# Kernel optimization log

Hardware: AMD Instinct MI355X
Metric: run time of the kernel (lower is better)

The kernel has to match this reference:

```python
import jax, jax.numpy as jnp
import numpy as np

EPS = 1e-5  # torch.nn.LayerNorm default
NUM_HEADS = 8


def _layernorm(x, g, b):
    mu = jnp.mean(x, axis=-1, keepdims=True)
    var = jnp.mean((x - mu) ** 2, axis=-1, keepdims=True)
    return (x - mu) * jax.lax.rsqrt(var + EPS) * g + b


def setup_inputs() -> dict:
    key = jax.random.key(0)
    ks = jax.random.split(key, 8)
    B, S, D = 4, 2048, 512
    scale = 0.02
    return {
        'x': jax.random.normal(ks[0], (B, S, D), dtype=jnp.float32),
        'gene_types': jax.random.randint(ks[1], (B, S), 0, 2),
        'tf_g': jnp.ones((D,), jnp.float32), 'tf_b': jnp.zeros((D,), jnp.float32),
        'tg_g': jnp.ones((D,), jnp.float32), 'tg_b': jnp.zeros((D,), jnp.float32),
        'in_proj_w': jax.random.normal(ks[2], (3 * D, D), dtype=jnp.float32) * scale,
        'in_proj_b': jnp.zeros((3 * D,), jnp.float32),
        'out_proj_w': jax.random.normal(ks[3], (D, D), dtype=jnp.float32) * scale,
        'out_proj_b': jnp.zeros((D,), jnp.float32),
        'w1': jax.random.normal(ks[4], (D // 2, D), dtype=jnp.float32) * scale,
        'b1': jnp.zeros((D // 2,), jnp.float32),
        'w2': jax.random.normal(ks[5], (1, D // 2), dtype=jnp.float32) * scale,
        'b2': jnp.zeros((1,), jnp.float32),
    }


def reference(x, gene_types, tf_g, tf_b, tg_g, tg_b,
              in_proj_w, in_proj_b, out_proj_w, out_proj_b,
              w1, b1, w2, b2):
    B, S, D = x.shape
    H = NUM_HEADS
    HD = D // H
    # --- vectorized per-token conditional LayerNorm (gene_type 0 -> tf, 1 -> target, else passthrough) ---
    gt = gene_types[..., None]
    xn = jnp.where(gt == 0, _layernorm(x, tf_g, tf_b),
                   jnp.where(gt == 1, _layernorm(x, tg_g, tg_b), x))
    # --- multi-head self-attention (torch MultiheadAttention, batch_first) ---
    qkv = xn @ in_proj_w.T + in_proj_b            # [B,S,3D]
    q, k, v = jnp.split(qkv, 3, axis=-1)
    to_heads = lambda t: t.reshape(B, S, H, HD).transpose(0, 2, 1, 3)  # [B,H,S,HD]
    q, k, v = to_heads(q), to_heads(k), to_heads(v)
    scores = jnp.einsum('bhqd,bhkd->bhqk', q, k) / jnp.sqrt(jnp.float32(HD))
    attn = jax.nn.softmax(scores, axis=-1)
    o = jnp.einsum('bhqk,bhkd->bhqd', attn, v)
    o = o.transpose(0, 2, 1, 3).reshape(B, S, D)
    o = o @ out_proj_w.T + out_proj_b
    xr = xn + o                                    # residual
    # --- regulatory strength gate: Linear -> SiLU -> Linear -> Sigmoid ---
    h = jax.nn.silu(xr @ w1.T + b1)                # [B,S,D/2]
    strength = jax.nn.sigmoid(h @ w2.T + b2)       # [B,S,1]
    return xr * strength
```

## Files before the change

kernel.cpp:

```cpp
#include <hip/hip_runtime.h>

typedef __bf16 bf16;
typedef __bf16 bf16x4_t __attribute__((ext_vector_type(4)));
typedef __bf16 bf16x8_t __attribute__((ext_vector_type(8)));
typedef float f32x4_t __attribute__((ext_vector_type(4)));

#define MFMA16(a, b, c) __builtin_amdgcn_mfma_f32_16x16x32_bf16(a, b, c, 0, 0, 0)

static __device__ __forceinline__ f32x4_t mfma_k16(bf16x4_t a, bf16x4_t b, f32x4_t c) {
#if __has_builtin(__builtin_amdgcn_mfma_f32_16x16x16bf16_1k)
    typedef short s16x4_t __attribute__((ext_vector_type(4)));
    return __builtin_amdgcn_mfma_f32_16x16x16bf16_1k(
        __builtin_bit_cast(s16x4_t, a), __builtin_bit_cast(s16x4_t, b), c, 0, 0, 0);
#else
    bf16x8_t az = {}, bz = {};
    az[0] = a[0]; az[1] = a[1]; az[2] = a[2]; az[3] = a[3];
    bz[0] = b[0]; bz[1] = b[1]; bz[2] = b[2]; bz[3] = b[3];
    return MFMA16(az, bz, c);
#endif
}

__global__ __launch_bounds__(256) void castln_k(const float* __restrict__ Wqkv,
                                                const float* __restrict__ Wout,
                                                const float* __restrict__ W1,
                                                bf16* __restrict__ wq,
                                                bf16* __restrict__ wo,
                                                bf16* __restrict__ w1b,
                                                const float* __restrict__ x,
                                                const int* __restrict__ gt,
                                                const float* __restrict__ tfg,
                                                const float* __restrict__ tfb,
                                                const float* __restrict__ tgg,
                                                const float* __restrict__ tgb,
                                                bf16* __restrict__ xn) {
    if (blockIdx.x < 4608) {
        int i = blockIdx.x * 256 + threadIdx.x;
        if (i < 786432) wq[i] = (bf16)Wqkv[i];
        else if (i < 1048576) wo[i - 786432] = (bf16)Wout[i - 786432];
        else if (i < 1179648) w1b[i - 1048576] = (bf16)W1[i - 1048576];
        return;
    }
    int wid = threadIdx.x >> 6, lane = threadIdx.x & 63;
    int t = (blockIdx.x - 4608) * 4 + wid;
    const float4* xr = (const float4*)(x + (size_t)t * 512);
    float4 a = xr[lane * 2], b = xr[lane * 2 + 1];
    float s = (a.x + a.y) + (a.z + a.w) + (b.x + b.y) + (b.z + b.w);
    float sq = a.x * a.x + a.y * a.y + a.z * a.z + a.w * a.w +
               b.x * b.x + b.y * b.y + b.z * b.z + b.w * b.w;
    for (int m = 1; m < 64; m <<= 1) {
        s += __shfl_xor(s, m, 64);
        sq += __shfl_xor(sq, m, 64);
    }
    float mean = s * (1.f / 512.f);
    float var = fmaxf(sq * (1.f / 512.f) - mean * mean, 0.f);
    float rstd = rsqrtf(var + 1e-5f);
    int g = gt[t];
    float4 o0, o1;
    if (g < 2) {
        const float4* gp = (const float4*)(g ? tgg : tfg);
        const float4* bp = (const float4*)(g ? tgb : tfb);
        float4 g0 = gp[lane * 2], g1 = gp[lane * 2 + 1];
        float4 b0 = bp[lane * 2], b1 = bp[lane * 2 + 1];
        o0.x = (a.x - mean) * rstd * g0.x + b0.x;
        o0.y = (a.y - mean) * rstd * g0.y + b0.y;
        o0.z = (a.z - mean) * rstd * g0.z + b0.z;
        o0.w = (a.w - mean) * rstd * g0.w + b0.w;
        o1.x = (b.x - mean) * rstd * g1.x + b1.x;
        o1.y = (b.y - mean) * rstd * g1.y + b1.y;
        o1.z = (b.z - mean) * rstd * g1.z + b1.z;
        o1.w = (b.w - mean) * rstd * g1.w + b1.w;
    } else {
        o0 = a; o1 = b;
    }
    bf16* xo = xn + (size_t)t * 512 + lane * 8;
    bf16x4_t p0, p1;
    p0[0] = (bf16)o0.x; p0[1] = (bf16)o0.y; p0[2] = (bf16)o0.z; p0[3] = (bf16)o0.w;
    p1[0] = (bf16)o1.x; p1[1] = (bf16)o1.y; p1[2] = (bf16)o1.z; p1[3] = (bf16)o1.w;
    *(bf16x4_t*)xo = p0;
    *(bf16x4_t*)(xo + 4) = p1;
}

__global__ __launch_bounds__(256) void gemmqkv_k(const bf16* __restrict__ A,
                                                 const bf16* __restrict__ B,
                                                 const float* __restrict__ bias,
                                                 bf16* __restrict__ q,
                                                 bf16* __restrict__ kk,
                                                 bf16* __restrict__ vt) {
    int m0 = blockIdx.x * 128, n0 = blockIdx.y * 128;
    int tid = threadIdx.x;
    int lane = tid & 63, w = tid >> 6;
    int quad = lane >> 4, l15 = lane & 15;
    int wm = (w >> 1) * 64, wn = (w & 1) * 64;
    __shared__ bf16 As[128 * 72];
    __shared__ bf16 Bs[128 * 72];
    f32x4_t acc[4][4] = {};
    int srow = tid >> 3, ssub = tid & 7;
    const bf16* Ab = A + (size_t)(m0 + srow) * 512 + ssub * 8;
    const bf16* Bb = B + (size_t)(n0 + srow) * 512 + ssub * 8;
    uint4 pa[4], pb[4];
    auto gload = [&](int s) {
        int k0 = s * 64;
#pragma unroll
        for (int i = 0; i < 4; ++i) {
            pa[i] = *(const uint4*)(Ab + (size_t)(i * 32) * 512 + k0);
            pb[i] = *(const uint4*)(Bb + (size_t)(i * 32) * 512 + k0);
        }
    };
    auto sstore = [&]() {
#pragma unroll
        for (int i = 0; i < 4; ++i) {
            *(uint4*)&As[(i * 32 + srow) * 72 + ssub * 8] = pa[i];
            *(uint4*)&Bs[(i * 32 + srow) * 72 + ssub * 8] = pb[i];
        }
    };
    gload(0);
    sstore();
    for (int s = 0; s < 8; ++s) {
        __syncthreads();
        if (s < 7) gload(s + 1);
#pragma unroll
        for (int ks = 0; ks < 2; ++ks) {
            bf16x8_t af[4], bfr[4];
            int koff = ks * 32 + quad * 8;
#pragma unroll
            for (int mt = 0; mt < 4; ++mt)
                af[mt] = *(const bf16x8_t*)&As[(wm + mt * 16 + l15) * 72 + koff];
#pragma unroll
            for (int nt = 0; nt < 4; ++nt)
                bfr[nt] = *(const bf16x8_t*)&Bs[(wn + nt * 16 + l15) * 72 + koff];
#pragma unroll
            for (int mt = 0; mt < 4; ++mt)
#pragma unroll
                for (int nt = 0; nt < 4; ++nt)
                    acc[mt][nt] = MFMA16(af[mt], bfr[nt], acc[mt][nt]);
        }
        __syncthreads();
        if (s < 7) sstore();
    }
#pragma unroll
    for (int mt = 0; mt < 4; ++mt) {
#pragma unroll
        for (int nt = 0; nt < 4; ++nt) {
            int gcol = n0 + wn + nt * 16 + l15;
            float bcol = bias[gcol];
#pragma unroll
            for (int r = 0; r < 4; ++r) {
                int grow = m0 + wm + mt * 16 + quad * 4 + r;
                float v = acc[mt][nt][r] + bcol;
                int which = gcol >> 9;
                int d = gcol & 511;
                int hh = d >> 6, hd = d & 63;
                int b = grow >> 11, ssi = grow & 2047;
                size_t bh = (size_t)(b * 8 + hh);
                if (which == 0) {
                    q[(bh * 2048 + ssi) * 64 + hd] = (bf16)(v * 0.180336880111f);
                } else if (which == 1) {
                    kk[(bh * 2048 + ssi) * 64 + hd] = (bf16)v;
                } else {
                    vt[(bh * 64 + hd) * 2048 + ssi] = (bf16)v;
                }
            }
        }
    }
}

__global__ __launch_bounds__(256) void attn_k(const bf16* __restrict__ q,
                                              const bf16* __restrict__ k,
                                              const bf16* __restrict__ vt,
                                              bf16* __restrict__ pO,
                                              float* __restrict__ pL) {
    int bh = blockIdx.y;
    int q0 = blockIdx.x * 128;
    int sz = blockIdx.z;
    const int kt0 = sz * 16;
    int tid = threadIdx.x;
    int lane = tid & 63, w = tid >> 6;
    int quad = lane >> 4, l15 = lane & 15;
    __shared__ bf16 Ks[64 * 72];
    __shared__ bf16 Vs[64 * 72];
    const bf16* qb = q + (size_t)bh * 2048 * 64;
    const bf16* kb = k + (size_t)bh * 2048 * 64;
    const bf16* vb = vt + (size_t)bh * 64 * 2048;
    bf16x8_t qf[2][2];
#pragma unroll
    for (int qt = 0; qt < 2; ++qt)
#pragma unroll
        for (int ks = 0; ks < 2; ++ks)
            qf[qt][ks] = *(const bf16x8_t*)(qb + (size_t)(q0 + w * 32 + qt * 16 + l15) * 64 + ks * 32 + quad * 8);
    bf16x4_t ones4;
#pragma unroll
    for (int i = 0; i < 4; ++i) ones4[i] = (bf16)1.0f;
    f32x4_t oacc[2][4] = {};
    f32x4_t lacc[2] = {};
    int srow = tid >> 3, ssub = tid & 7;
    uint4 pk[2], pv[2];
    auto gload = [&](int kt) {
        int kbase = kt * 64;
#pragma unroll
        for (int i = 0; i < 2; ++i) {
            int row = i * 32 + srow;
            pk[i] = *(const uint4*)(kb + (size_t)(kbase + row) * 64 + ssub * 8);
            pv[i] = *(const uint4*)(vb + (size_t)row * 2048 + kbase + ssub * 8);
        }
    };
    auto sstore = [&]() {
#pragma unroll
        for (int i = 0; i < 2; ++i) {
            int row = i * 32 + srow;
            *(uint4*)&Ks[row * 72 + ssub * 8] = pk[i];
            *(uint4*)&Vs[row * 72 + ssub * 8] = pv[i];
        }
    };
    gload(kt0);
    for (int kt = kt0; kt < kt0 + 16; ++kt) {
        __syncthreads();
        sstore();
        __syncthreads();
        if (kt + 1 < kt0 + 16) gload(kt + 1);
        f32x4_t sacc[4][2] = {};
#pragma unroll
        for (int ks = 0; ks < 2; ++ks) {
            int koff = ks * 32 + quad * 8;
            bf16x8_t kf[4];
#pragma unroll
            for (int nt = 0; nt < 4; ++nt)
                kf[nt] = *(const bf16x8_t*)&Ks[(nt * 16 + l15) * 72 + koff];
#pragma unroll
            for (int nt = 0; nt < 4; ++nt)
#pragma unroll
                for (int qt = 0; qt < 2; ++qt)
                    sacc[nt][qt] = MFMA16(kf[nt], qf[qt][ks], sacc[nt][qt]);
        }
        bf16x4_t pf[4][2];
#pragma unroll
        for (int nt = 0; nt < 4; ++nt)
#pragma unroll
            for (int qt = 0; qt < 2; ++qt)
#pragma unroll
                for (int r = 0; r < 4; ++r)
                    pf[nt][qt][r] = (bf16)exp2f(sacc[nt][qt][r]);
#pragma unroll
        for (int nt = 0; nt < 4; ++nt) {
            bf16x4_t vf[4];
#pragma unroll
            for (int dt = 0; dt < 4; ++dt)
                vf[dt] = *(const bf16x4_t*)&Vs[(dt * 16 + l15) * 72 + nt * 16 + quad * 4];
#pragma unroll
            for (int qt = 0; qt < 2; ++qt) {
#pragma unroll
                for (int dt = 0; dt < 4; ++dt)
                    oacc[qt][dt] = mfma_k16(pf[nt][qt], vf[dt], oacc[qt][dt]);
                lacc[qt] = mfma_k16(pf[nt][qt], ones4, lacc[qt]);
            }
        }
    }
    size_t obase = ((size_t)(sz * 32 + bh) * 2048 + q0);
#pragma unroll
    for (int qt = 0; qt < 2; ++qt)
#pragma unroll
        for (int r = 0; r < 4; ++r) {
            int row = w * 32 + qt * 16 + quad * 4 + r;
#pragma unroll
            for (int dt = 0; dt < 4; ++dt)
                pO[(obase + row) * 64 + dt * 16 + l15] = (bf16)oacc[qt][dt][r];
            if (l15 == 0) pL[obase + row] = lacc[qt][r];
        }
}

__global__ __launch_bounds__(256) void gemmo_k(const bf16* __restrict__ pO,
                                               const float* __restrict__ pL,
                                               const bf16* __restrict__ B,
                                               const float* __restrict__ bias,
                                               const bf16* __restrict__ xn,
                                               bf16* __restrict__ xrb,
                                               float* __restrict__ xrf) {
    int m0 = blockIdx.x * 128, n0 = blockIdx.y * 128;
    int tid = threadIdx.x;
    int lane = tid & 63, w = tid >> 6;
    int quad = lane >> 4, l15 = lane & 15;
    int wm = (w >> 1) * 64, wn = (w & 1) * 64;
    __shared__ bf16 As[128 * 72];
    __shared__ bf16 Bs[128 * 72];
    f32x4_t acc[4][4] = {};
    int srow = tid >> 3, ssub = tid & 7;
    const bf16* Bb = B + (size_t)(n0 + srow) * 512 + ssub * 8;
    bf16x8_t pa[4];
    uint4 pb[4];
    auto gload = [&](int s) {
        int k0 = s * 64;
#pragma unroll
        for (int i = 0; i < 4; ++i) {
            int t = m0 + i * 32 + srow;
            int b = t >> 11, ssi = t & 2047;
            size_t r0 = ((size_t)(b * 8 + s)) * 2048 + ssi;
            size_t r1 = ((size_t)(32 + b * 8 + s)) * 2048 + ssi;
            float inv = 1.f / (pL[r0] + pL[r1]);
            bf16x8_t a0 = *(const bf16x8_t*)(pO + r0 * 64 + ssub * 8);
            bf16x8_t a1 = *(const bf16x8_t*)(pO + r1 * 64 + ssub * 8);
            bf16x8_t c;
#pragma unroll
            for (int j = 0; j < 8; ++j) c[j] = (bf16)(((float)a0[j] + (float)a1[j]) * inv);
            pa[i] = c;
            pb[i] = *(const uint4*)(Bb + (size_t)(i * 32) * 512 + k0);
        }
    };
    auto sstore = [&]() {
#pragma unroll
        for (int i = 0; i < 4; ++i) {
            *(bf16x8_t*)&As[(i * 32 + srow) * 72 + ssub * 8] = pa[i];
            *(uint4*)&Bs[(i * 32 + srow) * 72 + ssub * 8] = pb[i];
        }
    };
    gload(0);
    sstore();
    for (int s = 0; s < 8; ++s) {
        __syncthreads();
        if (s < 7) gload(s + 1);
#pragma unroll
        for (int ks = 0; ks < 2; ++ks) {
            bf16x8_t af[4], bfr[4];
            int koff = ks * 32 + quad * 8;
#pragma unroll
            for (int mt = 0; mt < 4; ++mt)
                af[mt] = *(const bf16x8_t*)&As[(wm + mt * 16 + l15) * 72 + koff];
#pragma unroll
            for (int nt = 0; nt < 4; ++nt)
                bfr[nt] = *(const bf16x8_t*)&Bs[(wn + nt * 16 + l15) * 72 + koff];
#pragma unroll
            for (int mt = 0; mt < 4; ++mt)
#pragma unroll
                for (int nt = 0; nt < 4; ++nt)
                    acc[mt][nt] = MFMA16(af[mt], bfr[nt], acc[mt][nt]);
        }
        __syncthreads();
        if (s < 7) sstore();
    }
#pragma unroll
    for (int mt = 0; mt < 4; ++mt) {
#pragma unroll
        for (int nt = 0; nt < 4; ++nt) {
            int gcol = n0 + wn + nt * 16 + l15;
            float bcol = bias[gcol];
#pragma unroll
            for (int r = 0; r < 4; ++r) {
                int grow = m0 + wm + mt * 16 + quad * 4 + r;
                size_t idx = (size_t)grow * 512 + gcol;
                float xv = acc[mt][nt][r] + bcol + (float)xn[idx];
                xrf[idx] = xv;
                xrb[idx] = (bf16)xv;
            }
        }
    }
}

__global__ __launch_bounds__(256) void mlp_k(const bf16* __restrict__ A,
                                             const bf16* __restrict__ B,
                                             const float* __restrict__ b1,
                                             const float* __restrict__ w2,
                                             const float* __restrict__ b2,
                                             const float* __restrict__ xrf,
                                             float* __restrict__ out) {
    int m0 = blockIdx.x * 32;
    int tid = threadIdx.x;
    int lane = tid & 63, w = tid >> 6;
    int quad = lane >> 4, l15 = lane & 15;
    int wn = w * 64;
    __shared__ bf16 As[32 * 72];
    __shared__ bf16 Bs[256 * 72];
    __shared__ float red[4][32];
    __shared__ float st[32];
    f32x4_t acc[2][4] = {};
    int srow = tid >> 3, ssub = tid & 7;
    uint4 pa, pb[8];
    auto gload = [&](int s) {
        int k0 = s * 64;
        pa = *(const uint4*)(A + (size_t)(m0 + srow) * 512 + ssub * 8 + k0);
#pragma unroll
        for (int i = 0; i < 8; ++i)
            pb[i] = *(const uint4*)(B + (size_t)(i * 32 + srow) * 512 + ssub * 8 + k0);
    };
    auto sstore = [&]() {
        *(uint4*)&As[srow * 72 + ssub * 8] = pa;
#pragma unroll
        for (int i = 0; i < 8; ++i)
            *(uint4*)&Bs[(i * 32 + srow) * 72 + ssub * 8] = pb[i];
    };
    gload(0);
    sstore();
    for (int s = 0; s < 8; ++s) {
        __syncthreads();
        if (s < 7) gload(s + 1);
#pragma unroll
        for (int ks = 0; ks < 2; ++ks) {
            int koff = ks * 32 + quad * 8;
            bf16x8_t af[2], bfr[4];
#pragma unroll
            for (int mt = 0; mt < 2; ++mt)
                af[mt] = *(const bf16x8_t*)&As[(mt * 16 + l15) * 72 + koff];
#pragma unroll
            for (int nt = 0; nt < 4; ++nt)
                bfr[nt] = *(const bf16x8_t*)&Bs[(wn + nt * 16 + l15) * 72 + koff];
#pragma unroll
            for (int mt = 0; mt < 2; ++mt)
#pragma unroll
                for (int nt = 0; nt < 4; ++nt)
                    acc[mt][nt] = MFMA16(af[mt], bfr[nt], acc[mt][nt]);
        }
        __syncthreads();
        if (s < 7) sstore();
    }
    f32x4_t ds[2] = {};
#pragma unroll
    for (int mt = 0; mt < 2; ++mt)
#pragma unroll
        for (int nt = 0; nt < 4; ++nt) {
            int gcol = wn + nt * 16 + l15;
            float bb = b1[gcol], ww = w2[gcol];
#pragma unroll
            for (int r = 0; r < 4; ++r) {
                float v = acc[mt][nt][r] + bb;
                float sv = v / (1.f + __expf(-v));
                ds[mt][r] += sv * ww;
            }
        }
#pragma unroll
    for (int m = 1; m < 16; m <<= 1)
#pragma unroll
        for (int mt = 0; mt < 2; ++mt)
#pragma unroll
            for (int r = 0; r < 4; ++r) ds[mt][r] += __shfl_xor(ds[mt][r], m, 64);
    if (l15 == 0) {
#pragma unroll
        for (int mt = 0; mt < 2; ++mt)
#pragma unroll
            for (int r = 0; r < 4; ++r) red[w][mt * 16 + quad * 4 + r] = ds[mt][r];
    }
    __syncthreads();
    if (tid < 32) {
        float d = red[0][tid] + red[1][tid] + red[2][tid] + red[3][tid] + b2[0];
        st[tid] = 1.f / (1.f + __expf(-d));
    }
    __syncthreads();
    int row = tid >> 3, seg = tid & 7;
    float sr = st[row];
    const float4* x4 = (const float4*)(xrf + (size_t)(m0 + row) * 512);
    float4* o4 = (float4*)(out + (size_t)(m0 + row) * 512);
#pragma unroll
    for (int jj = 0; jj < 16; ++jj) {
        float4 xv = x4[jj * 8 + seg];
        float4 ov;
        ov.x = xv.x * sr; ov.y = xv.y * sr; ov.z = xv.z * sr; ov.w = xv.w * sr;
        o4[jj * 8 + seg] = ov;
    }
}

extern "C" void kernel_launch(void* const* d_in, const int* in_sizes, int n_in,
                              void* d_out, int out_size, void* d_ws, size_t ws_size,
                              hipStream_t stream) {
    const float* x    = (const float*)d_in[0];
    const int*   gt   = (const int*)d_in[1];
    const float* tfg  = (const float*)d_in[2];
    const float* tfb  = (const float*)d_in[3];
    const float* tgg  = (const float*)d_in[4];
    const float* tgb  = (const float*)d_in[5];
    const float* Wqkv = (const float*)d_in[6];
    const float* bqkv = (const float*)d_in[7];
    const float* Wout = (const float*)d_in[8];
    const float* bout = (const float*)d_in[9];
    const float* W1   = (const float*)d_in[10];
    const float* b1   = (const float*)d_in[11];
    const float* w2   = (const float*)d_in[12];
    const float* b2   = (const float*)d_in[13];
    float* out = (float*)d_out;
    char* ws = (char*)d_ws;

    const size_t MB = 1024 * 1024;
    bf16*  wq  = (bf16*)(ws + 0);
    bf16*  wo  = (bf16*)(ws + 1536 * 512 * 2);
    bf16*  w1b = (bf16*)(ws + (1536 + 512) * 512 * 2);
    float* pL  = (float*)(ws + 2304 * 512 * 2);
    bf16*  xn  = (bf16*)(ws + 4 * MB);
    bf16*  q   = (bf16*)(ws + 12 * MB);
    bf16*  xrb = (bf16*)(ws + 12 * MB);
    bf16*  kk  = (bf16*)(ws + 20 * MB);
    bf16*  vt  = (bf16*)(ws + 28 * MB);
    bf16*  pO  = (bf16*)(ws + 36 * MB);
    float* xrf = (float*)(ws + 52 * MB);

    castln_k<<<6656, 256, 0, stream>>>(Wqkv, Wout, W1, wq, wo, w1b,
                                       x, gt, tfg, tfb, tgg, tgb, xn);
    gemmqkv_k<<<dim3(64, 12), 256, 0, stream>>>(xn, wq, bqkv, q, kk, vt);
    attn_k<<<dim3(16, 32, 2), 256, 0, stream>>>(q, kk, vt, pO, pL);
    gemmo_k<<<dim3(64, 4), 256, 0, stream>>>(pO, pL, wo, bout, xn, xrb, xrf);
    mlp_k<<<256, 256, 0, stream>>>(xrb, w1b, b1, w2, b2, xrf, out);
    (void)in_sizes; (void)n_in; (void)out_size; (void)ws_size;
}
```

Measured before the change: 336.1 us.

## Stage softmax probabilities through LDS for K=32 MFMA and add separate V transpose

Attention now computes scores as Q·K^T and writes the exp2 probabilities to a shared-memory tile. They are read back as 8-wide fragments so the PV product and the row-sum both use the 16x16x32 bf16 MFMA instead of the 16x16x16 variant. The QKV GEMM now writes V in row-major layout with contiguous stores, and a new kernel transposes it into vt with coalesced writes through LDS, replacing the strided scattered stores. This trades an extra kernel launch, an extra V read/write pass, and extra LDS traffic and synchronisation-free LDS round-trips for fewer, larger MFMAs and better-coalesced global stores.

```diff
diff --git a/kernel.cpp b/kernel.cpp
--- a/kernel.cpp
+++ b/kernel.cpp
@@ -6,19 +6,6 @@
 typedef float f32x4_t __attribute__((ext_vector_type(4)));
 
 #define MFMA16(a, b, c) __builtin_amdgcn_mfma_f32_16x16x32_bf16(a, b, c, 0, 0, 0)
-
-static __device__ __forceinline__ f32x4_t mfma_k16(bf16x4_t a, bf16x4_t b, f32x4_t c) {
-#if __has_builtin(__builtin_amdgcn_mfma_f32_16x16x16bf16_1k)
-    typedef short s16x4_t __attribute__((ext_vector_type(4)));
-    return __builtin_amdgcn_mfma_f32_16x16x16bf16_1k(
-        __builtin_bit_cast(s16x4_t, a), __builtin_bit_cast(s16x4_t, b), c, 0, 0, 0);
-#else
-    bf16x8_t az = {}, bz = {};
-    az[0] = a[0]; az[1] = a[1]; az[2] = a[2]; az[3] = a[3];
-    bz[0] = b[0]; bz[1] = b[1]; bz[2] = b[2]; bz[3] = b[3];
-    return MFMA16(az, bz, c);
-#endif
-}
 
 __global__ __launch_bounds__(256) void castln_k(const float* __restrict__ Wqkv,
                                                 const float* __restrict__ Wout,
@@ -85,7 +72,7 @@
                                                  const float* __restrict__ bias,
                                                  bf16* __restrict__ q,
                                                  bf16* __restrict__ kk,
-                                                 bf16* __restrict__ vt) {
+                                                 bf16* __restrict__ vv) {
     int m0 = blockIdx.x * 128, n0 = blockIdx.y * 128;
     int tid = threadIdx.x;
     int lane = tid & 63, w = tid >> 6;
@@ -152,16 +139,36 @@
                 int hh = d >> 6, hd = d & 63;
                 int b = grow >> 11, ssi = grow & 2047;
                 size_t bh = (size_t)(b * 8 + hh);
+                size_t idx = (bh * 2048 + ssi) * 64 + hd;
                 if (which == 0) {
-                    q[(bh * 2048 + ssi) * 64 + hd] = (bf16)(v * 0.180336880111f);
+                    q[idx] = (bf16)(v * 0.180336880111f);
                 } else if (which == 1) {
-                    kk[(bh * 2048 + ssi) * 64 + hd] = (bf16)v;
+                    kk[idx] = (bf16)v;
                 } else {
-                    vt[(bh * 64 + hd) * 2048 + ssi] = (bf16)v;
+                    vv[idx] = (bf16)v;
                 }
             }
         }
     }
+}
+
+__global__ __launch_bounds__(256) void vtrans_k(const bf16* __restrict__ v,
+                                                bf16* __restrict__ vt) {
+    int bh = blockIdx.y;
+    int s0 = blockIdx.x * 64;
+    __shared__ bf16 Ls[64][72];
+    int tid = threadIdx.x;
+    int row = tid >> 2, seg = tid & 3;
+    const bf16* vb = v + ((size_t)bh * 2048 + s0 + row) * 64 + seg * 16;
+    *(uint4*)&Ls[row][seg * 16] = *(const uint4*)vb;
+    *(uint4*)&Ls[row][seg * 16 + 8] = *(const uint4*)(vb + 8);
+    __syncthreads();
+    bf16 tmp[16];
+#pragma unroll
+    for (int i = 0; i < 16; ++i) tmp[i] = Ls[seg * 16 + i][row];
+    bf16* dst = vt + ((size_t)bh * 64 + row) * 2048 + s0 + seg * 16;
+    *(uint4*)dst = *(uint4*)&tmp[0];
+    *(uint4*)(dst + 8) = *(uint4*)&tmp[8];
 }
 
 __global__ __launch_bounds__(256) void attn_k(const bf16* __restrict__ q,
@@ -172,35 +179,36 @@
     int bh = blockIdx.y;
     int q0 = blockIdx.x * 128;
     int sz = blockIdx.z;
-    const int kt0 = sz * 16;
+    int kt0 = sz * 16;
     int tid = threadIdx.x;
     int lane = tid & 63, w = tid >> 6;
     int quad = lane >> 4, l15 = lane & 15;
     __shared__ bf16 Ks[64 * 72];
     __shared__ bf16 Vs[64 * 72];
+    __shared__ bf16 Ps[128 * 72];
     const bf16* qb = q + (size_t)bh * 2048 * 64;
     const bf16* kb = k + (size_t)bh * 2048 * 64;
     const bf16* vb = vt + (size_t)bh * 64 * 2048;
     bf16x8_t qf[2][2];
 #pragma unroll
-    for (int qt = 0; qt < 2; ++qt)
+    for (int mt = 0; mt < 2; ++mt)
 #pragma unroll
         for (int ks = 0; ks < 2; ++ks)
-            qf[qt][ks] = *(const bf16x8_t*)(qb + (size_t)(q0 + w * 32 + qt * 16 + l15) * 64 + ks * 32 + quad * 8);
-    bf16x4_t ones4;
-#pragma unroll
-    for (int i = 0; i < 4; ++i) ones4[i] = (bf16)1.0f;
+            qf[mt][ks] = *(const bf16x8_t*)(qb + (size_t)(q0 + w * 32 + mt * 16 + l15) * 64 + ks * 32 + quad * 8);
+    bf16x8_t ones8;
+#pragma unroll
+    for (int i = 0; i < 8; ++i) ones8[i] = (bf16)1.0f;
     f32x4_t oacc[2][4] = {};
     f32x4_t lacc[2] = {};
     int srow = tid >> 3, ssub = tid & 7;
-    uint4 pk[2], pv[2];
+    uint4 pk[2], pw[2];
     auto gload = [&](int kt) {
         int kbase = kt * 64;
 #pragma unroll
         for (int i = 0; i < 2; ++i) {
             int row = i * 32 + srow;
             pk[i] = *(const uint4*)(kb + (size_t)(kbase + row) * 64 + ssub * 8);
-            pv[i] = *(const uint4*)(vb + (size_t)row * 2048 + kbase + ssub * 8);
+            pw[i] = *(const uint4*)(vb + (size_t)row * 2048 + kbase + ssub * 8);
         }
     };
     auto sstore = [&]() {
@@ -208,7 +216,7 @@
         for (int i = 0; i < 2; ++i) {
             int row = i * 32 + srow;
             *(uint4*)&Ks[row * 72 + ssub * 8] = pk[i];
-            *(uint4*)&Vs[row * 72 + ssub * 8] = pv[i];
+            *(uint4*)&Vs[row * 72 + ssub * 8] = pw[i];
         }
     };
     gload(kt0);
@@ -217,7 +225,7 @@
         sstore();
         __syncthreads();
         if (kt + 1 < kt0 + 16) gload(kt + 1);
-        f32x4_t sacc[4][2] = {};
+        f32x4_t sacc[2][4] = {};
 #pragma unroll
         for (int ks = 0; ks < 2; ++ks) {
             int koff = ks * 32 + quad * 8;
@@ -226,44 +234,47 @@
             for (int nt = 0; nt < 4; ++nt)
                 kf[nt] = *(const bf16x8_t*)&Ks[(nt * 16 + l15) * 72 + koff];
 #pragma unroll
-            for (int nt = 0; nt < 4; ++nt)
-#pragma unroll
-                for (int qt = 0; qt < 2; ++qt)
-                    sacc[nt][qt] = MFMA16(kf[nt], qf[qt][ks], sacc[nt][qt]);
-        }
-        bf16x4_t pf[4][2];
-#pragma unroll
-        for (int nt = 0; nt < 4; ++nt)
-#pragma unroll
-            for (int qt = 0; qt < 2; ++qt)
+            for (int mt = 0; mt < 2; ++mt)
+#pragma unroll
+                for (int nt = 0; nt < 4; ++nt)
+                    sacc[mt][nt] = MFMA16(qf[mt][ks], kf[nt], sacc[mt][nt]);
+        }
+#pragma unroll
+        for (int mt = 0; mt < 2; ++mt)
+#pragma unroll
+            for (int nt = 0; nt < 4; ++nt)
 #pragma unroll
                 for (int r = 0; r < 4; ++r)
-                    pf[nt][qt][r] = (bf16)exp2f(sacc[nt][qt][r]);
-#pragma unroll
-        for (int nt = 0; nt < 4; ++nt) {
-            bf16x4_t vf[4];
-#pragma unroll
-            for (int dt = 0; dt < 4; ++dt)
-                vf[dt] = *(const bf16x4_t*)&Vs[(dt * 16 + l15) * 72 + nt * 16 + quad * 4];
-#pragma unroll
-            for (int qt = 0; qt < 2; ++qt) {
-#pragma unroll
-                for (int dt = 0; dt < 4; ++dt)
-                    oacc[qt][dt] = mfma_k16(pf[nt][qt], vf[dt], oacc[qt][dt]);
-                lacc[qt] = mfma_k16(pf[nt][qt], ones4, lacc[qt]);
+                    Ps[(w * 32 + mt * 16 + quad * 4 + r) * 72 + nt * 16 + l15] = (bf16)exp2f(sacc[mt][nt][r]);
+#pragma unroll
+        for (int ks = 0; ks < 2; ++ks) {
+            int koff = ks * 32 + quad * 8;
+            bf16x8_t pf[2], vf[4];
+#pragma unroll
+            for (int mt = 0; mt < 2; ++mt)
+                pf[mt] = *(const bf16x8_t*)&Ps[(w * 32 + mt * 16 + l15) * 72 + koff];
+#pragma unroll
+            for (int nt = 0; nt < 4; ++nt)
+                vf[nt] = *(const bf16x8_t*)&Vs[(nt * 16 + l15) * 72 + koff];
+#pragma unroll
+            for (int mt = 0; mt < 2; ++mt) {
+#pragma unroll
+                for (int nt = 0; nt < 4; ++nt)
+                    oacc[mt][nt] = MFMA16(pf[mt], vf[nt], oacc[mt][nt]);
+                lacc[mt] = MFMA16(pf[mt], ones8, lacc[mt]);
             }
         }
     }
     size_t obase = ((size_t)(sz * 32 + bh) * 2048 + q0);
 #pragma unroll
-    for (int qt = 0; qt < 2; ++qt)
+    for (int mt = 0; mt < 2; ++mt)
 #pragma unroll
         for (int r = 0; r < 4; ++r) {
-            int row = w * 32 + qt * 16 + quad * 4 + r;
-#pragma unroll
-            for (int dt = 0; dt < 4; ++dt)
-                pO[(obase + row) * 64 + dt * 16 + l15] = (bf16)oacc[qt][dt][r];
-            if (l15 == 0) pL[obase + row] = lacc[qt][r];
+            int row = w * 32 + mt * 16 + quad * 4 + r;
+#pragma unroll
+            for (int nt = 0; nt < 4; ++nt)
+                pO[(obase + row) * 64 + nt * 16 + l15] = (bf16)oacc[mt][nt][r];
+            if (l15 == 0) pL[obase + row] = lacc[mt][r];
         }
 }
 
@@ -483,13 +494,15 @@
     bf16*  q   = (bf16*)(ws + 12 * MB);
     bf16*  xrb = (bf16*)(ws + 12 * MB);
     bf16*  kk  = (bf16*)(ws + 20 * MB);
-    bf16*  vt  = (bf16*)(ws + 28 * MB);
-    bf16*  pO  = (bf16*)(ws + 36 * MB);
-    float* xrf = (float*)(ws + 52 * MB);
+    bf16*  vv  = (bf16*)(ws + 28 * MB);
+    bf16*  vt  = (bf16*)(ws + 36 * MB);
+    float* xrf = (float*)(ws + 28 * MB);
+    bf16*  pO  = (bf16*)(ws + 44 * MB);
 
     castln_k<<<6656, 256, 0, stream>>>(Wqkv, Wout, W1, wq, wo, w1b,
                                        x, gt, tfg, tfb, tgg, tgb, xn);
-    gemmqkv_k<<<dim3(64, 12), 256, 0, stream>>>(xn, wq, bqkv, q, kk, vt);
+    gemmqkv_k<<<dim3(64, 12), 256, 0, stream>>>(xn, wq, bqkv, q, kk, vv);
+    vtrans_k<<<dim3(32, 32), 256, 0, stream>>>(vv, vt);
     attn_k<<<dim3(16, 32, 2), 256, 0, stream>>>(q, kk, vt, pO, pL);
     gemmo_k<<<dim3(64, 4), 256, 0, stream>>>(pO, pL, wo, bout, xn, xrb, xrf);
     mlp_k<<<256, 256, 0, stream>>>(xrb, w1b, b1, w2, b2, xrf, out);
```

Result: no change. 331.7 us (-1.3%).
